# Optimization experiments

Hardware: AMD Instinct MI355X
Metric: run time of the kernel (lower is better)

Reference implementation:

```python
import jax, jax.numpy as jnp
import numpy as np

B, TE, TD, DE, DD = 4, 256, 256, 512, 512


def setup_inputs() -> dict:
    key = jax.random.key(0)
    k1, k2, k3, k4, k5 = jax.random.split(key, 5)
    return {
        "encoder_outputs": jax.random.normal(k1, (B, TE, DE), dtype=jnp.float32),
        "decoder_outputs": jax.random.normal(k2, (B, TD, DD), dtype=jnp.float32),
        "U_a": jax.random.normal(k3, (DE, DE), dtype=jnp.float32) * 0.05,
        "W_a": jax.random.normal(k4, (DD, DE), dtype=jnp.float32) * 0.05,
        "V_a": jax.random.normal(k5, (DE,), dtype=jnp.float32) * 0.05,
    }


def reference(encoder_outputs, decoder_outputs, U_a, W_a, V_a):
    # U_a_dot_h: [B, Te, De] -- precomputed once, as in the original
    Uh = jnp.einsum("bec,cd->bed", encoder_outputs, U_a)
    # W_a_dot_s for all decoder steps at once (original loops over t): [B, Td, De]
    Ws = jnp.einsum("btc,cd->btd", decoder_outputs, W_a)
    # additive energies: tanh(Uh + Ws) . V_a -> [B, Td, Te]
    e = jnp.einsum("bted,d->bte", jnp.tanh(Uh[:, None, :, :] + Ws[:, :, None, :]), V_a)
    attn = jax.nn.softmax(e, axis=-1)  # softmax over encoder timesteps
    # context: weighted sum of encoder outputs -> [B, Td, De]
    context = jnp.einsum("bte,bec->btc", attn, encoder_outputs)
    return context, attn
```

## Files before the change

### kernel.cpp

```cpp
#include <hip/hip_runtime.h>

#define B_    4
#define TE_   256
#define TD_   256
#define DE_   512
#define K_    512

typedef __attribute__((ext_vector_type(8))) short bf16x8;
typedef __attribute__((ext_vector_type(4))) float f32x4;

#define C1F 2.8853900817779268f

__device__ __forceinline__ ushort f2bf(float x) {
  uint u = __float_as_uint(x);
  return (ushort)((u + 0x7fffu + ((u >> 16) & 1u)) >> 16);
}
__device__ __forceinline__ float bf2f(ushort h) {
  return __uint_as_float(((uint)h) << 16);
}
__device__ __forceinline__ float exp2_fast(float x) {
  float r;
  asm("v_exp_f32 %0, %1" : "=v"(r) : "v"(x));
  return r;
}

__global__ __launch_bounds__(256) void conv_hilo(
    const float* __restrict__ enc, const float* __restrict__ dec,
    ushort* __restrict__ ehi, ushort* __restrict__ elo,
    ushort* __restrict__ dhi, ushort* __restrict__ dlo) {
  const float* in = blockIdx.y ? dec : enc;
  ushort* hi = blockIdx.y ? dhi : ehi;
  ushort* lo = blockIdx.y ? dlo : elo;
  int i = (blockIdx.x * 256 + threadIdx.x) * 4;
  float4 v = *(const float4*)&in[i];
  ushort4 h, l;
  h.x = f2bf(v.x); l.x = f2bf(v.x - bf2f(h.x));
  h.y = f2bf(v.y); l.y = f2bf(v.y - bf2f(h.y));
  h.z = f2bf(v.z); l.z = f2bf(v.z - bf2f(h.z));
  h.w = f2bf(v.w); l.w = f2bf(v.w - bf2f(h.w));
  *(ushort4*)&hi[i] = h;
  *(ushort4*)&lo[i] = l;
}

__global__ __launch_bounds__(256) void conv_bt(
    const float* __restrict__ Ua, const float* __restrict__ Wa,
    ushort* __restrict__ uhi, ushort* __restrict__ ulo,
    ushort* __restrict__ whi, ushort* __restrict__ wlo) {
  const float* in = blockIdx.z ? Wa : Ua;
  ushort* thi = blockIdx.z ? whi : uhi;
  ushort* tlo = blockIdx.z ? wlo : ulo;
  __shared__ float tile[64][65];
  int k0 = blockIdx.y * 64, n0 = blockIdx.x * 64;
  int tid = threadIdx.x;
#pragma unroll
  for (int i = 0; i < 16; ++i) {
    int idx = tid + i * 256;
    int r = idx >> 6, c = idx & 63;
    tile[r][c] = in[(size_t)(k0 + r) * 512 + n0 + c];
  }
  __syncthreads();
#pragma unroll
  for (int i = 0; i < 16; ++i) {
    int idx = tid + i * 256;
    int rn = idx >> 6, ck = idx & 63;
    float x = tile[ck][rn] * C1F;
    ushort h = f2bf(x);
    size_t o = (size_t)(n0 + rn) * 512 + k0 + ck;
    thi[o] = h;
    tlo[o] = f2bf(x - bf2f(h));
  }
}

__global__ __launch_bounds__(256) void gemm_mfma(
    const ushort* __restrict__ ehi, const ushort* __restrict__ elo,
    const ushort* __restrict__ dhi, const ushort* __restrict__ dlo,
    const ushort* __restrict__ uhi, const ushort* __restrict__ ulo,
    const ushort* __restrict__ whi, const ushort* __restrict__ wlo,
    float* __restrict__ UhT, float* __restrict__ Ws) {
  const ushort *Ahi, *Alo, *Bhi, *Blo;
  int bid = blockIdx.x, bm, bn;
  if (blockIdx.z == 0) {
    Ahi = uhi; Alo = ulo; Bhi = ehi; Blo = elo;
    bn = (bid & 31) * 32; bm = (bid >> 5) * 32;
  } else {
    Ahi = dhi; Alo = dlo; Bhi = whi; Blo = wlo;
    bn = (bid & 15) * 32; bm = (bid >> 4) * 32;
  }
  __shared__ __align__(16) ushort Ah[32 * 40], Al[32 * 40];
  __shared__ __align__(16) ushort Bh[32 * 40], Bl[32 * 40];
  int tid = threadIdx.x, lane = tid & 63, w = tid >> 6;
  int srow = tid >> 3, sko = (tid & 7) * 4;
  size_t aoff = (size_t)(bm + srow) * K_ + sko;
  size_t boff = (size_t)(bn + srow) * K_ + sko;
  int sdst = srow * 40 + sko;
  int wm = w >> 1, wn = w & 1;
  int frow = lane & 15, fch = (lane >> 4) * 8;
  int ra = (wm * 16 + frow) * 40 + fch;
  int rb = (wn * 16 + frow) * 40 + fch;
  uint2 rah = *(const uint2*)&Ahi[aoff];
  uint2 ral = *(const uint2*)&Alo[aoff];
  uint2 rbh = *(const uint2*)&Bhi[boff];
  uint2 rbl = *(const uint2*)&Blo[boff];
  f32x4 acc = {};
  for (int ks = 0; ks < 16; ++ks) {
    __syncthreads();
    *(uint2*)&Ah[sdst] = rah;
    *(uint2*)&Al[sdst] = ral;
    *(uint2*)&Bh[sdst] = rbh;
    *(uint2*)&Bl[sdst] = rbl;
    __syncthreads();
    if (ks < 15) {
      size_t ko = (size_t)(ks + 1) * 32;
      rah = *(const uint2*)&Ahi[aoff + ko];
      ral = *(const uint2*)&Alo[aoff + ko];
      rbh = *(const uint2*)&Bhi[boff + ko];
      rbl = *(const uint2*)&Blo[boff + ko];
    }
    bf16x8 ah = *(const bf16x8*)&Ah[ra], al = *(const bf16x8*)&Al[ra];
    bf16x8 bh = *(const bf16x8*)&Bh[rb], bl = *(const bf16x8*)&Bl[rb];
    acc = __builtin_amdgcn_mfma_f32_16x16x32_bf16(ah, bh, acc, 0, 0, 0);
    acc = __builtin_amdgcn_mfma_f32_16x16x32_bf16(ah, bl, acc, 0, 0, 0);
    acc = __builtin_amdgcn_mfma_f32_16x16x32_bf16(al, bh, acc, 0, 0, 0);
  }
  int m0 = bm + wm * 16 + (lane >> 4) * 4;
  int n0 = bn + wn * 16 + (lane & 15);
  if (blockIdx.z == 0) {
    float* cb = UhT + (size_t)(n0 >> 8) * 131072 + (size_t)m0 * 256 + (n0 & 255);
#pragma unroll
    for (int r = 0; r < 4; ++r) cb[(size_t)r * 256] = acc[r];
  } else {
    float* cb = Ws + (size_t)m0 * 512 + n0;
#pragma unroll
    for (int r = 0; r < 4; ++r) cb[(size_t)r * 512] = acc[r];
  }
}

__global__ __launch_bounds__(512) void fused_attn(
    const float* __restrict__ enc, const float* __restrict__ UhT,
    const float* __restrict__ Ws, const float* __restrict__ Va,
    float* __restrict__ out_ctx, float* __restrict__ out_attn) {
  int bt = blockIdx.x;
  int b  = bt >> 7;
  int t0 = (bt & 127) * 2;
  __shared__ float ws0_s[DE_], ws1_s[DE_], mv_s[DE_];
  __shared__ float e_s[2][TE_];
  __shared__ float att2[TE_ * 2];
  __shared__ float redm[2][4], reds[2][4];
  int tid = threadIdx.x, lane = tid & 63, w = tid >> 6;

  const float* wsr = Ws + (size_t)(b * TD_ + t0) * DE_;
  ws0_s[tid] = wsr[tid];
  ws1_s[tid] = wsr[DE_ + tid];
  mv_s[tid]  = -2.0f * Va[tid];
  __syncthreads();

  int half = lane >> 5, sub = lane & 31;
  int e = w * 32 + sub;
  const float* up = UhT + (size_t)b * 131072 + (size_t)half * 65536 + e;
  int dbase = half * 256;
  float acc0 = 0.f, acc1 = 0.f;
#pragma unroll 8
  for (int d0 = 0; d0 < 256; d0 += 4) {
    int dd = dbase + d0;
    float4 wv0 = *(const float4*)&ws0_s[dd];
    float4 wv1 = *(const float4*)&ws1_s[dd];
    float4 mv4 = *(const float4*)&mv_s[dd];
#pragma unroll
    for (int j = 0; j < 4; ++j) {
      float u = up[(d0 + j) * 256];
      float w0 = j == 0 ? wv0.x : j == 1 ? wv0.y : j == 2 ? wv0.z : wv0.w;
      float w1 = j == 0 ? wv1.x : j == 1 ? wv1.y : j == 2 ? wv1.z : wv1.w;
      float mv = j == 0 ? mv4.x : j == 1 ? mv4.y : j == 2 ? mv4.z : mv4.w;
      float r0 = __builtin_amdgcn_rcpf(1.0f + exp2_fast(u + w0));
      float r1 = __builtin_amdgcn_rcpf(1.0f + exp2_fast(u + w1));
      acc0 = fmaf(mv, r0, acc0);
      acc1 = fmaf(mv, r1, acc1);
    }
  }
  acc0 += __shfl_xor(acc0, 32);
  acc1 += __shfl_xor(acc1, 32);
  if (lane < 32) { e_s[0][e] = acc0; e_s[1][e] = acc1; }
  __syncthreads();

  int t = tid >> 8, col = tid & 255;
  float x = e_s[t][col];
  float m = x;
#pragma unroll
  for (int off = 32; off; off >>= 1) m = fmaxf(m, __shfl_xor(m, off));
  if (lane == 0) redm[t][w & 3] = m;
  __syncthreads();
  m = fmaxf(fmaxf(redm[t][0], redm[t][1]), fmaxf(redm[t][2], redm[t][3]));
  float p = __expf(x - m);
  float s = p;
#pragma unroll
  for (int off = 32; off; off >>= 1) s += __shfl_xor(s, off);
  if (lane == 0) reds[t][w & 3] = s;
  __syncthreads();
  s = reds[t][0] + reds[t][1] + reds[t][2] + reds[t][3];
  float a = p * __builtin_amdgcn_rcpf(s);
  att2[col * 2 + t] = a;
  out_attn[(size_t)(b * TD_ + t0 + t) * TE_ + col] = a;
  __syncthreads();

  const float* enc_b = enc + (size_t)b * TE_ * DE_;
  float c0 = 0.f, c1 = 0.f;
#pragma unroll 4
  for (int ee = 0; ee < TE_; ++ee) {
    float2 av = *(const float2*)&att2[ee * 2];
    float xv = enc_b[(size_t)ee * DE_ + tid];
    c0 = fmaf(av.x, xv, c0);
    c1 = fmaf(av.y, xv, c1);
  }
  float* ctx0 = out_ctx + (size_t)(b * TD_ + t0) * DE_;
  ctx0[tid]       = c0;
  ctx0[DE_ + tid] = c1;
}

extern "C" void kernel_launch(void* const* d_in, const int* in_sizes, int n_in,
                              void* d_out, int out_size, void* d_ws, size_t ws_size,
                              hipStream_t stream) {
  const float* enc = (const float*)d_in[0];
  const float* dec = (const float*)d_in[1];
  const float* Ua  = (const float*)d_in[2];
  const float* Wa  = (const float*)d_in[3];
  const float* Va  = (const float*)d_in[4];

  float* out_ctx  = (float*)d_out;
  float* out_attn = out_ctx + (size_t)B_ * TD_ * DE_;

  char* wsp = (char*)d_ws;
  float* UhT = (float*)wsp;             wsp += (size_t)B_ * DE_ * TE_ * 4;
  float* Wsm = (float*)wsp;             wsp += (size_t)B_ * TD_ * DE_ * 4;
  ushort* ehi = (ushort*)wsp;           wsp += (size_t)B_ * TE_ * DE_ * 2;
  ushort* elo = (ushort*)wsp;           wsp += (size_t)B_ * TE_ * DE_ * 2;
  ushort* dhi = (ushort*)wsp;           wsp += (size_t)B_ * TD_ * DE_ * 2;
  ushort* dlo = (ushort*)wsp;           wsp += (size_t)B_ * TD_ * DE_ * 2;
  ushort* uhi = (ushort*)wsp;           wsp += (size_t)K_ * DE_ * 2;
  ushort* ulo = (ushort*)wsp;           wsp += (size_t)K_ * DE_ * 2;
  ushort* whi = (ushort*)wsp;           wsp += (size_t)K_ * DE_ * 2;
  ushort* wlo = (ushort*)wsp;           wsp += (size_t)K_ * DE_ * 2;

  conv_hilo<<<dim3(512, 2), 256, 0, stream>>>(enc, dec, ehi, elo, dhi, dlo);
  conv_bt<<<dim3(8, 8, 2), 256, 0, stream>>>(Ua, Wa, uhi, ulo, whi, wlo);
  gemm_mfma<<<dim3(512, 1, 2), 256, 0, stream>>>(
      ehi, elo, dhi, dlo, uhi, ulo, whi, wlo, UhT, Wsm);
  fused_attn<<<512, 512, 0, stream>>>(enc, UhT, Wsm, Va, out_ctx, out_attn);
}
```

Measured before the change: 129.7 us.

## Use single-wave LDS-free GEMM tiles and float4-vectorized energy loop

The GEMM kernel drops shared-memory staging and its barriers. Each 64-thread block now computes a full 32x32 tile with four MFMA accumulators, loading bf16 fragments straight from global memory. The fused attention kernel changes its energy loop so each lane reads a float4 of four encoder columns of UhT per d-step instead of scalar loads. Its smem Ws/Va vectors are padded to avoid bank conflicts, and partial sums are reduced across eight d-groups with shuffles. The cost is redundant global fragment loads in the GEMM, since there is no LDS reuse, and more shuffle reductions in the energy stage.

```diff
diff --git a/kernel.cpp b/kernel.cpp
--- a/kernel.cpp
+++ b/kernel.cpp
@@ -71,7 +71,7 @@
   }
 }
 
-__global__ __launch_bounds__(256) void gemm_mfma(
+__global__ __launch_bounds__(64) void gemm_mfma(
     const ushort* __restrict__ ehi, const ushort* __restrict__ elo,
     const ushort* __restrict__ dhi, const ushort* __restrict__ dlo,
     const ushort* __restrict__ uhi, const ushort* __restrict__ ulo,
@@ -86,53 +86,52 @@
     Ahi = dhi; Alo = dlo; Bhi = whi; Blo = wlo;
     bn = (bid & 15) * 32; bm = (bid >> 4) * 32;
   }
-  __shared__ __align__(16) ushort Ah[32 * 40], Al[32 * 40];
-  __shared__ __align__(16) ushort Bh[32 * 40], Bl[32 * 40];
-  int tid = threadIdx.x, lane = tid & 63, w = tid >> 6;
-  int srow = tid >> 3, sko = (tid & 7) * 4;
-  size_t aoff = (size_t)(bm + srow) * K_ + sko;
-  size_t boff = (size_t)(bn + srow) * K_ + sko;
-  int sdst = srow * 40 + sko;
-  int wm = w >> 1, wn = w & 1;
-  int frow = lane & 15, fch = (lane >> 4) * 8;
-  int ra = (wm * 16 + frow) * 40 + fch;
-  int rb = (wn * 16 + frow) * 40 + fch;
-  uint2 rah = *(const uint2*)&Ahi[aoff];
-  uint2 ral = *(const uint2*)&Alo[aoff];
-  uint2 rbh = *(const uint2*)&Bhi[boff];
-  uint2 rbl = *(const uint2*)&Blo[boff];
-  f32x4 acc = {};
-  for (int ks = 0; ks < 16; ++ks) {
-    __syncthreads();
-    *(uint2*)&Ah[sdst] = rah;
-    *(uint2*)&Al[sdst] = ral;
-    *(uint2*)&Bh[sdst] = rbh;
-    *(uint2*)&Bl[sdst] = rbl;
-    __syncthreads();
-    if (ks < 15) {
-      size_t ko = (size_t)(ks + 1) * 32;
-      rah = *(const uint2*)&Ahi[aoff + ko];
-      ral = *(const uint2*)&Alo[aoff + ko];
-      rbh = *(const uint2*)&Bhi[boff + ko];
-      rbl = *(const uint2*)&Blo[boff + ko];
+  int lane = threadIdx.x;
+  int frow = lane & 15, fk = (lane >> 4) * 8;
+  size_t ao = (size_t)(bm + frow) * K_ + fk;
+  size_t bo = (size_t)(bn + frow) * K_ + fk;
+  const ushort* pah0 = Ahi + ao; const ushort* pah1 = pah0 + 16 * K_;
+  const ushort* pal0 = Alo + ao; const ushort* pal1 = pal0 + 16 * K_;
+  const ushort* pbh0 = Bhi + bo; const ushort* pbh1 = pbh0 + 16 * K_;
+  const ushort* pbl0 = Blo + bo; const ushort* pbl1 = pbl0 + 16 * K_;
+  f32x4 a00 = {}, a01 = {}, a10 = {}, a11 = {};
+#pragma unroll 2
+  for (int k0 = 0; k0 < K_; k0 += 32) {
+    bf16x8 ah0 = *(const bf16x8*)&pah0[k0], ah1 = *(const bf16x8*)&pah1[k0];
+    bf16x8 al0 = *(const bf16x8*)&pal0[k0], al1 = *(const bf16x8*)&pal1[k0];
+    bf16x8 bh0 = *(const bf16x8*)&pbh0[k0], bh1 = *(const bf16x8*)&pbh1[k0];
+    bf16x8 bl0 = *(const bf16x8*)&pbl0[k0], bl1 = *(const bf16x8*)&pbl1[k0];
+    a00 = __builtin_amdgcn_mfma_f32_16x16x32_bf16(ah0, bh0, a00, 0, 0, 0);
+    a01 = __builtin_amdgcn_mfma_f32_16x16x32_bf16(ah0, bh1, a01, 0, 0, 0);
+    a10 = __builtin_amdgcn_mfma_f32_16x16x32_bf16(ah1, bh0, a10, 0, 0, 0);
+    a11 = __builtin_amdgcn_mfma_f32_16x16x32_bf16(ah1, bh1, a11, 0, 0, 0);
+    a00 = __builtin_amdgcn_mfma_f32_16x16x32_bf16(ah0, bl0, a00, 0, 0, 0);
+    a01 = __builtin_amdgcn_mfma_f32_16x16x32_bf16(ah0, bl1, a01, 0, 0, 0);
+    a10 = __builtin_amdgcn_mfma_f32_16x16x32_bf16(ah1, bl0, a10, 0, 0, 0);
+    a11 = __builtin_amdgcn_mfma_f32_16x16x32_bf16(ah1, bl1, a11, 0, 0, 0);
+    a00 = __builtin_amdgcn_mfma_f32_16x16x32_bf16(al0, bh0, a00, 0, 0, 0);
+    a01 = __builtin_amdgcn_mfma_f32_16x16x32_bf16(al0, bh1, a01, 0, 0, 0);
+    a10 = __builtin_amdgcn_mfma_f32_16x16x32_bf16(al1, bh0, a10, 0, 0, 0);
+    a11 = __builtin_amdgcn_mfma_f32_16x16x32_bf16(al1, bh1, a11, 0, 0, 0);
+  }
+  int crow = (lane >> 4) * 4, ccol = lane & 15;
+#pragma unroll
+  for (int i = 0; i < 2; ++i)
+#pragma unroll
+    for (int j = 0; j < 2; ++j) {
+      const f32x4& acc = i == 0 ? (j == 0 ? a00 : a01) : (j == 0 ? a10 : a11);
+      int m0 = bm + i * 16 + crow;
+      int n0 = bn + j * 16 + ccol;
+      if (blockIdx.z == 0) {
+        float* cb = UhT + (size_t)(n0 >> 8) * 131072 + (size_t)m0 * 256 + (n0 & 255);
+#pragma unroll
+        for (int r = 0; r < 4; ++r) cb[(size_t)r * 256] = acc[r];
+      } else {
+        float* cb = Ws + (size_t)m0 * 512 + n0;
+#pragma unroll
+        for (int r = 0; r < 4; ++r) cb[(size_t)r * 512] = acc[r];
+      }
     }
-    bf16x8 ah = *(const bf16x8*)&Ah[ra], al = *(const bf16x8*)&Al[ra];
-    bf16x8 bh = *(const bf16x8*)&Bh[rb], bl = *(const bf16x8*)&Bl[rb];
-    acc = __builtin_amdgcn_mfma_f32_16x16x32_bf16(ah, bh, acc, 0, 0, 0);
-    acc = __builtin_amdgcn_mfma_f32_16x16x32_bf16(ah, bl, acc, 0, 0, 0);
-    acc = __builtin_amdgcn_mfma_f32_16x16x32_bf16(al, bh, acc, 0, 0, 0);
-  }
-  int m0 = bm + wm * 16 + (lane >> 4) * 4;
-  int n0 = bn + wn * 16 + (lane & 15);
-  if (blockIdx.z == 0) {
-    float* cb = UhT + (size_t)(n0 >> 8) * 131072 + (size_t)m0 * 256 + (n0 & 255);
-#pragma unroll
-    for (int r = 0; r < 4; ++r) cb[(size_t)r * 256] = acc[r];
-  } else {
-    float* cb = Ws + (size_t)m0 * 512 + n0;
-#pragma unroll
-    for (int r = 0; r < 4; ++r) cb[(size_t)r * 512] = acc[r];
-  }
 }
 
 __global__ __launch_bounds__(512) void fused_attn(
@@ -142,44 +141,51 @@
   int bt = blockIdx.x;
   int b  = bt >> 7;
   int t0 = (bt & 127) * 2;
-  __shared__ float ws0_s[DE_], ws1_s[DE_], mv_s[DE_];
+  __shared__ float ws0_s[520], ws1_s[520], mv_s[520];
   __shared__ float e_s[2][TE_];
   __shared__ float att2[TE_ * 2];
   __shared__ float redm[2][4], reds[2][4];
   int tid = threadIdx.x, lane = tid & 63, w = tid >> 6;
 
   const float* wsr = Ws + (size_t)(b * TD_ + t0) * DE_;
-  ws0_s[tid] = wsr[tid];
-  ws1_s[tid] = wsr[DE_ + tid];
-  mv_s[tid]  = -2.0f * Va[tid];
-  __syncthreads();
-
-  int half = lane >> 5, sub = lane & 31;
-  int e = w * 32 + sub;
-  const float* up = UhT + (size_t)b * 131072 + (size_t)half * 65536 + e;
-  int dbase = half * 256;
-  float acc0 = 0.f, acc1 = 0.f;
+  int pd0 = tid + (tid >> 6);
+  ws0_s[pd0] = wsr[tid];
+  ws1_s[pd0] = wsr[DE_ + tid];
+  mv_s[pd0]  = -2.0f * Va[tid];
+  __syncthreads();
+
+  int dg = lane >> 3, qlow = lane & 7;
+  int q = w * 8 + qlow;
+  const float* up = UhT + (size_t)b * 131072 + (size_t)dg * 64 * 256 + q * 4;
+  int pbase = dg * 65;
+  float a0[4] = {}, a1[4] = {};
 #pragma unroll 8
-  for (int d0 = 0; d0 < 256; d0 += 4) {
-    int dd = dbase + d0;
-    float4 wv0 = *(const float4*)&ws0_s[dd];
-    float4 wv1 = *(const float4*)&ws1_s[dd];
-    float4 mv4 = *(const float4*)&mv_s[dd];
+  for (int i = 0; i < 64; ++i) {
+    float4 u4 = *(const float4*)&up[(size_t)i * 256];
+    float w0 = ws0_s[pbase + i];
+    float w1 = ws1_s[pbase + i];
+    float mv = mv_s[pbase + i];
 #pragma unroll
     for (int j = 0; j < 4; ++j) {
-      float u = up[(d0 + j) * 256];
-      float w0 = j == 0 ? wv0.x : j == 1 ? wv0.y : j == 2 ? wv0.z : wv0.w;
-      float w1 = j == 0 ? wv1.x : j == 1 ? wv1.y : j == 2 ? wv1.z : wv1.w;
-      float mv = j == 0 ? mv4.x : j == 1 ? mv4.y : j == 2 ? mv4.z : mv4.w;
-      float r0 = __builtin_amdgcn_rcpf(1.0f + exp2_fast(u + w0));
-      float r1 = __builtin_amdgcn_rcpf(1.0f + exp2_fast(u + w1));
-      acc0 = fmaf(mv, r0, acc0);
-      acc1 = fmaf(mv, r1, acc1);
+      float u = j == 0 ? u4.x : j == 1 ? u4.y : j == 2 ? u4.z : u4.w;
+      a0[j] = fmaf(mv, __builtin_amdgcn_rcpf(1.0f + exp2_fast(u + w0)), a0[j]);
+      a1[j] = fmaf(mv, __builtin_amdgcn_rcpf(1.0f + exp2_fast(u + w1)), a1[j]);
     }
   }
-  acc0 += __shfl_xor(acc0, 32);
-  acc1 += __shfl_xor(acc1, 32);
-  if (lane < 32) { e_s[0][e] = acc0; e_s[1][e] = acc1; }
+#pragma unroll
+  for (int j = 0; j < 4; ++j) {
+#pragma unroll
+    for (int off = 8; off <= 32; off <<= 1) {
+      a0[j] += __shfl_xor(a0[j], off);
+      a1[j] += __shfl_xor(a1[j], off);
+    }
+  }
+  if (dg == 0) {
+    float4 v0 = make_float4(a0[0], a0[1], a0[2], a0[3]);
+    float4 v1 = make_float4(a1[0], a1[1], a1[2], a1[3]);
+    *(float4*)&e_s[0][q * 4] = v0;
+    *(float4*)&e_s[1][q * 4] = v1;
+  }
   __syncthreads();
 
   int t = tid >> 8, col = tid & 255;
@@ -242,7 +248,7 @@
 
   conv_hilo<<<dim3(512, 2), 256, 0, stream>>>(enc, dec, ehi, elo, dhi, dlo);
   conv_bt<<<dim3(8, 8, 2), 256, 0, stream>>>(Ua, Wa, uhi, ulo, whi, wlo);
-  gemm_mfma<<<dim3(512, 1, 2), 256, 0, stream>>>(
+  gemm_mfma<<<dim3(512, 1, 2), 64, 0, stream>>>(
       ehi, elo, dhi, dlo, uhi, ulo, whi, wlo, UhT, Wsm);
   fused_attn<<<512, 512, 0, stream>>>(enc, UhT, Wsm, Va, out_ctx, out_attn);
 }
```

After: 131.5 us. About the same (+1.4%).
